# Kernel tuning notes

Measured on AMD Instinct MI355X. Metric: run time of the kernel, lower is better.

The kernel has to match this reference:

```python
import jax, jax.numpy as jnp
import numpy as np

B, T, C, H, NT = 1, 1024, 768, 12, 8
D = C // H  # 64
POWER_ITERS = 4
DP_TEMP = 0.8
ESR_GAMMA = 0.02
ESR_ALPHA = 0.1


def rmsnorm(x, w, eps=1e-6):
    rms = jax.lax.rsqrt(jnp.mean(x * x, axis=-1, keepdims=True) + eps)
    return x * rms * w


def setup_inputs():
    key = jax.random.key(0)
    k0, k1, k2 = jax.random.split(key, 3)
    return {
        "x": jax.random.normal(k0, (B, T, C), jnp.float32),
        "W_qkvg": jax.random.normal(k1, (4 * C, C), jnp.float32) * 0.02,
        "W_out": jax.random.normal(k2, (C, C), jnp.float32) * 0.02,
        "lam": jnp.float32(1.5),
        "log_tau": -0.5 * jnp.ones((H, NT), jnp.float32),
        "logit_w": jnp.zeros((H, NT), jnp.float32),
        "beta": 1.5 * jnp.ones((H,), jnp.float32),
        "out_scale": jnp.ones((H,), jnp.float32),
        "dp_scale": jnp.ones((H,), jnp.float32),
        "logk_scale": jnp.ones((H,), jnp.float32),
        "dt_logit": jnp.float32(np.log(1.0 / 1e-8)),  # dt=1.0 -> logit = log(dt/(1-dt+1e-8))
        "g_norm_w": jnp.ones((D,), jnp.float32),
    }


def reference(x, W_qkvg, W_out, lam, log_tau, logit_w, beta, out_scale,
              dp_scale, logk_scale, dt_logit, g_norm_w):
    # qkvg projection and head split
    qkvg = x @ W_qkvg.T                                    # [B,T,4C]
    q, k, v, g = jnp.split(qkvg, 4, axis=-1)
    to_heads = lambda t: t.reshape(B, T, H, D).transpose(0, 2, 1, 3)  # [B,H,T,D]
    q, k, v, g = map(to_heads, (q, k, v, g))
    g = rmsnorm(g, g_norm_w)

    # pairwise squared distance ||g_i - g_j||^2
    g2 = jnp.sum(g * g, axis=-1)                           # [B,H,T]
    s = jnp.maximum(g2[..., :, None] + g2[..., None, :]
                    - 2.0 * jnp.einsum('bhid,bhjd->bhij', g, g), 0.0)  # [B,H,T,T]

    # fractional log-kernel: logsumexp_t[-(beta/2) log1p(s/(4 tau_t)) + log w_t]
    tau = jnp.maximum(jnp.exp(log_tau), 1e-6)              # [H,NT]
    w = jax.nn.softmax(logit_w, axis=-1)                   # [H,NT]
    beta_c = jnp.clip(beta, 0.5, 2.5)                      # [H]
    log_k_per = -(beta_c[None, :, None, None, None] / 2.0) * jnp.log1p(
        s[:, :, None] / (4.0 * tau[None, :, :, None, None]))          # [B,H,NT,T,T]
    logK = jax.nn.logsumexp(log_k_per + jnp.log(w + 1e-12)[None, :, :, None, None], axis=2)
    logK = logK * logk_scale[None, :, None, None]

    # dot-product scores
    dp = jnp.einsum('bhid,bhjd->bhij', q, k) * (dp_scale[None, :, None, None]
                                                / (np.sqrt(D) * DP_TEMP))

    # causal Markov normalize: blend, mask, stable row-softmax
    mask = jnp.tril(jnp.ones((T, T), bool))[None, None]    # [1,1,T,T]
    blended = lam * dp + (1.0 - lam) * logK
    blended = jnp.where(mask, blended, -jnp.inf)
    mx = jnp.max(blended, axis=-1, keepdims=True)
    mx = jnp.where(jnp.isfinite(mx), mx, 0.0)
    Kmat = jnp.exp(jnp.maximum(blended - mx, -60.0)) * mask
    P = Kmat / jnp.maximum(Kmat.sum(-1, keepdims=True), 1e-12)

    # power iteration for left stationary pi with full-support teleport
    pi0 = jnp.full((B, H, 1, T), 1.0 / T, P.dtype)
    def step(pi, _):
        p = (1.0 - ESR_GAMMA) * (pi @ P) + ESR_GAMMA / T
        p = p / jnp.maximum(p.sum(-1, keepdims=True), 1e-12)
        return p, None
    pi, _ = jax.lax.scan(step, pi0, None, length=POWER_ITERS)
    pi = jax.lax.stop_gradient(pi[..., 0, :])              # [B,H,T] (detached)

    # causal approximation to additive reversibilization
    P_adj = (pi[..., None, :] / jnp.maximum(pi[..., :, None], 1e-12)) \
            * jnp.swapaxes(P, -1, -2)                      # P*_ij = (pi_j/pi_i) P_ji
    P_rev = 0.5 * (P + P_adj) * mask
    P_rev = P_rev / jnp.maximum(P_rev.sum(-1, keepdims=True), 1e-12)

    dt = jax.nn.sigmoid(dt_logit)
    alpha = ESR_ALPHA * dt                                  # scale_alpha_by_dt=True
    P_fin = (1.0 - alpha) * P + alpha * P_rev

    y = (P_fin @ v) * out_scale[None, :, None, None]       # [B,H,T,D]
    y = y.transpose(0, 2, 1, 3).reshape(B, T, C)
    return y @ W_out.T
```

## Files before the change

kernel.cpp:

```cpp
#include <hip/hip_runtime.h>
#include <math.h>

#define TSEQ 1024
#define CD   768
#define HN   12
#define DD   64
#define CH   2

#define OFF_QH     0
#define OFF_KH     393216
#define OFF_GH     786432
#define OFF_VHT    1179648
#define OFF_VH     1572864
#define OFF_G2     1966080
#define OFF_YB     1978368
#define OFF_CONSTS 2371584
#define OFF_OPART  2372096
#define OFF_LS     8663552
#define OFF_PD     8761856
#define OFF_XB     8774144
#define OFF_WQB    9167360
#define OFF_WOB    10347008

#define NG_X  98304
#define NG_WQ 294912
#define NG_WO 73728

typedef __bf16 bf16x8 __attribute__((ext_vector_type(8)));
typedef float  f32x4  __attribute__((ext_vector_type(4)));
typedef unsigned short u16x8 __attribute__((ext_vector_type(8)));
typedef unsigned short u16x4 __attribute__((ext_vector_type(4)));

__device__ inline unsigned short f2bf(float f) {
  unsigned int u = __float_as_uint(f);
  return (unsigned short)((u + 0x7fffu + ((u >> 16) & 1u)) >> 16);
}
__device__ inline float bf2f(unsigned short u) {
  return __uint_as_float((unsigned)u << 16);
}


__global__ __launch_bounds__(256) void convert_kernel(
    const float* __restrict__ x, const float* __restrict__ wq,
    const float* __restrict__ wo, unsigned short* __restrict__ swzA,
    unsigned short* __restrict__ swzWQ, unsigned short* __restrict__ swzWO,
    const float* __restrict__ lam_p, const float* __restrict__ log_tau,
    const float* __restrict__ logit_w, const float* __restrict__ beta,
    const float* __restrict__ out_scale, const float* __restrict__ dp_scale,
    const float* __restrict__ logk_scale, const float* __restrict__ dt_logit,
    float* __restrict__ consts) {
  if (blockIdx.x == 0 && threadIdx.x < 64) {
    int h = threadIdx.x;
    if (h == 0) {
      float dt = 1.0f / (1.0f + __expf(-dt_logit[0]));
      consts[288] = 0.1f * dt;
    }
    if (h < HN) {
      float lam = lam_p[0];
      float* c = consts + h * 24;
      c[0] = lam * dp_scale[h] * (1.0f / 6.4f);
      c[1] = (1.0f - lam) * logk_scale[h];
      float b = fminf(fmaxf(beta[h], 0.5f), 2.5f);
      c[2] = 0.5f * b;
      c[3] = out_scale[h];
      float m = -1e30f;
      float lw[8];
      bool uni = true;
      for (int t = 0; t < 8; t++) {
        lw[t] = logit_w[h * 8 + t];
        m = fmaxf(m, lw[t]);
        if (log_tau[h * 8 + t] != log_tau[h * 8] || lw[t] != lw[0]) uni = false;
      }
      float s = 0.f;
      float e[8];
      for (int t = 0; t < 8; t++) { e[t] = __expf(lw[t] - m); s += e[t]; }
      for (int t = 0; t < 8; t++) {
        float w = e[t] / s;
        c[12 + t] = log2f(w + 1e-12f);
        float tau = fmaxf(__expf(log_tau[h * 8 + t]), 1e-6f);
        c[4 + t] = 1.0f / (4.0f * tau);
      }
      c[20] = uni ? 1.0f : 8.0f;
    }
  }
  int g = blockIdx.x * 256 + threadIdx.x;
  const float* src;
  unsigned short* dst;
  int lg;
  if (g < NG_X) { src = x; dst = swzA; lg = g; }
  else if (g < NG_X + NG_WQ) { src = wq; dst = swzWQ; lg = g - NG_X; }
  else if (g < NG_X + NG_WQ + NG_WO) { src = wo; dst = swzWO; lg = g - NG_X - NG_WQ; }
  else return;
  int lane = lg & 63;
  int kb = (lg >> 6) % 24;
  int t16 = lg / (64 * 24);
  int row = t16 * 16 + (lane & 15);
  int col = kb * 32 + (lane >> 4) * 8;
  const float* s = &src[(size_t)row * 768 + col];
  float4 a = *(const float4*)s;
  float4 b = *(const float4*)(s + 4);
  u16x8 u;
  u[0] = f2bf(a.x); u[1] = f2bf(a.y); u[2] = f2bf(a.z); u[3] = f2bf(a.w);
  u[4] = f2bf(b.x); u[5] = f2bf(b.y); u[6] = f2bf(b.z); u[7] = f2bf(b.w);
  *(u16x8*)&dst[(size_t)lg * 8] = u;
}

__global__ __launch_bounds__(256) void gemm_frag_qkvg(
    const unsigned short* __restrict__ swzA, const unsigned short* __restrict__ swzB,
    const float* __restrict__ consts, const float* __restrict__ g_norm_w,
    unsigned short* __restrict__ qh, unsigned short* __restrict__ kh,
    unsigned short* __restrict__ gh, unsigned short* __restrict__ vh,
    unsigned short* __restrict__ vhT, float* __restrict__ g2) {
  __shared__ __align__(16) unsigned short Ls[64 * 72];
  int t = threadIdx.x, lane = t & 63, w = t >> 6;
  int quad = lane >> 4, tx = lane & 15;
  int bid = blockIdx.x;
  int c = (bid & 7) * 96 + (bid >> 3);
  int ntile = c >> 4;
  int ybk = c & 15;
  int nt0 = ntile * 4;
  int mt0 = ybk * 4 + w;
  int mrow0 = mt0 * 16;

  f32x4 acc[4] = {};
#pragma unroll 4
  for (int kb = 0; kb < 24; kb++) {
    bf16x8 a0 = *(const bf16x8*)&swzA[((size_t)(mt0 * 24 + kb) * 64 + lane) * 8];
#pragma unroll
    for (int ni = 0; ni < 4; ni++) {
      bf16x8 b = *(const bf16x8*)&swzB[((size_t)((nt0 + ni) * 24 + kb) * 64 + lane) * 8];
      acc[ni] = __builtin_amdgcn_mfma_f32_16x16x32_bf16(a0, b, acc[ni], 0, 0, 0);
    }
  }

  int typ = ntile / 12;
  int h = ntile % 12;
  unsigned short* Lw = Ls + w * (16 * 72);

  if (typ == 3) {
    float gw4[4];
#pragma unroll
    for (int ni = 0; ni < 4; ni++) gw4[ni] = g_norm_w[ni * 16 + tx];
#pragma unroll
    for (int reg = 0; reg < 4; reg++) {
      float s1 = acc[0][reg] * acc[0][reg] + acc[1][reg] * acc[1][reg]
               + acc[2][reg] * acc[2][reg] + acc[3][reg] * acc[3][reg];
#pragma unroll
      for (int m = 1; m < 16; m <<= 1) s1 += __shfl_xor(s1, m, 64);
      float rms = rsqrtf(s1 * (1.f / 64.f) + 1e-6f);
      int rl = quad * 4 + reg;
      float s2 = 0.f;
#pragma unroll
      for (int ni = 0; ni < 4; ni++) {
        float v = acc[ni][reg] * rms * gw4[ni];
        unsigned short us = f2bf(v);
        Lw[rl * 72 + ni * 16 + tx] = us;
        float vb = bf2f(us);
        s2 += vb * vb;
      }
#pragma unroll
      for (int m = 1; m < 16; m <<= 1) s2 += __shfl_xor(s2, m, 64);
      if (tx == 0) g2[h * 1024 + mrow0 + rl] = s2;
    }
#pragma unroll
    for (int rep = 0; rep < 2; rep++) {
      int idx = rep * 64 + lane;
      int r = idx >> 3, cc = (idx & 7) * 8;
      *(u16x8*)&gh[(size_t)(h * 1024 + mrow0 + r) * 64 + cc] = *(const u16x8*)&Lw[r * 72 + cc];
    }
  } else {
    float sc = (typ == 0) ? consts[h * 24] * 1.44269504089f : 1.0f;
#pragma unroll
    for (int ni = 0; ni < 4; ni++)
#pragma unroll
      for (int reg = 0; reg < 4; reg++) {
        int rl = quad * 4 + reg;
        Lw[rl * 72 + ni * 16 + tx] = f2bf(acc[ni][reg] * sc);
      }
    unsigned short* dst = (typ == 0) ? qh : ((typ == 1) ? kh : vh);
#pragma unroll
    for (int rep = 0; rep < 2; rep++) {
      int idx = rep * 64 + lane;
      int r = idx >> 3, cc = (idx & 7) * 8;
      *(u16x8*)&dst[(size_t)(h * 1024 + mrow0 + r) * 64 + cc] = *(const u16x8*)&Lw[r * 72 + cc];
    }
    if (typ == 2) {
#pragma unroll
      for (int rep = 0; rep < 2; rep++) {
        int idx = rep * 64 + lane;
        int d = idx >> 1, rc = (idx & 1) * 8;
        u16x8 u;
#pragma unroll
        for (int j = 0; j < 8; j++) u[j] = Lw[(rc + j) * 72 + d];
        *(u16x8*)&vhT[(size_t)(h * 64 + d) * 1024 + mrow0 + rc] = u;
      }
    }
  }
}

__global__ __launch_bounds__(256) void gemm_frag_out(
    const unsigned short* __restrict__ swzA, const unsigned short* __restrict__ swzB,
    float* __restrict__ Cm) {
  int t = threadIdx.x, lane = t & 63, w = t >> 6;
  int quad = lane >> 4, tx = lane & 15;
  int n0 = blockIdx.x * 32;
  int nt0 = blockIdx.x * 2;
  int mt0 = blockIdx.y * 4 + w;

  f32x4 acc[2] = {};
#pragma unroll 4
  for (int kb = 0; kb < 24; kb++) {
    bf16x8 a0 = *(const bf16x8*)&swzA[((size_t)(mt0 * 24 + kb) * 64 + lane) * 8];
#pragma unroll
    for (int ni = 0; ni < 2; ni++) {
      bf16x8 b = *(const bf16x8*)&swzB[((size_t)((nt0 + ni) * 24 + kb) * 64 + lane) * 8];
      acc[ni] = __builtin_amdgcn_mfma_f32_16x16x32_bf16(a0, b, acc[ni], 0, 0, 0);
    }
  }
#pragma unroll
  for (int ni = 0; ni < 2; ni++)
#pragma unroll
    for (int reg = 0; reg < 4; reg++) {
      int row = mt0 * 16 + quad * 4 + reg;
      Cm[(size_t)row * CD + n0 + ni * 16 + tx] = acc[ni][reg];
    }
}

__global__ __launch_bounds__(256, 4) void flash_kernel(
    const unsigned short* __restrict__ qh, const unsigned short* __restrict__ kh,
    const unsigned short* __restrict__ gh, const unsigned short* __restrict__ vhT,
    const float* __restrict__ g2, const float* __restrict__ consts,
    float* __restrict__ Opart, float* __restrict__ lsp, float* __restrict__ pdp) {
  int bid = blockIdx.x;
  int cc0 = (bid & 7) * 108 + (bid >> 3);
  int h = cc0 / 72;
  int uu = 71 - (cc0 % 72);
  int it = 0, rem = uu;
  for (it = 0; it < 16; ++it) {
    int nc = (it + 2) >> 1;
    if (rem < nc) break;
    rem -= nc;
  }
  int njt = it + 1;
  int jt0 = rem * CH;
  int jt1 = (jt0 + CH < njt) ? (jt0 + CH) : njt;
  bool owns_diag = (jt1 == njt);
  int i0 = it * 64;
  int t = threadIdx.x;
  int lane = t & 63, w = t >> 6;
  int quad = lane >> 4, tx = lane & 15;

  __shared__ __align__(16) unsigned short Ks[64 * 72];
  __shared__ __align__(16) unsigned short Gjs[64 * 72];
  __shared__ __align__(16) unsigned short Vt[64 * 72];
  __shared__ __align__(16) __bf16 psh[64 * 72];
  __shared__ float g2i[64], g2j[64], pdiag[64];

  const float* ch = consts + h * 24;
  float lkc = ch[1], bh2 = ch[2];
  int ntt = (int)ch[20];
  float i4t0 = ch[4];
  float cfold = -lkc * bh2;
  float m2i4 = -2.0f * i4t0;
  float g2s = (ntt == 1) ? i4t0 : 1.0f;

  int r4 = t >> 2, cb = (t & 3) * 16;
  int rowb = w * 16 + quad * 4;

  u16x8 pk0, pk1, pg0, pg1, pv0, pv1;
  float pg2 = 0.f;
  {
    int j0 = jt0 * 64;
    const unsigned short* kp = &kh[(size_t)(h * 1024 + j0 + r4) * 64 + cb];
    const unsigned short* gp = &gh[(size_t)(h * 1024 + j0 + r4) * 64 + cb];
    const unsigned short* vp = &vhT[(size_t)(h * 64 + r4) * 1024 + j0 + cb];
    pk0 = *(const u16x8*)kp; pk1 = *(const u16x8*)(kp + 8);
    pg0 = *(const u16x8*)gp; pg1 = *(const u16x8*)(gp + 8);
    pv0 = *(const u16x8*)vp; pv1 = *(const u16x8*)(vp + 8);
    if (t < 64) pg2 = g2[h * 1024 + j0 + t];
  }

  {
    const unsigned short* qp = &qh[(size_t)(h * 1024 + i0 + r4) * 64 + cb];
    const unsigned short* gp = &gh[(size_t)(h * 1024 + i0 + r4) * 64 + cb];
    *(u16x8*)&Ks[r4 * 72 + cb] = *(const u16x8*)qp;
    *(u16x8*)&Ks[r4 * 72 + cb + 8] = *(const u16x8*)(qp + 8);
    *(u16x8*)&Gjs[r4 * 72 + cb] = *(const u16x8*)gp;
    *(u16x8*)&Gjs[r4 * 72 + cb + 8] = *(const u16x8*)(gp + 8);
  }
  if (t < 64) { g2i[t] = g2[h * 1024 + i0 + t]; pdiag[t] = 0.f; }
  __syncthreads();

  bf16x8 aq[2], ag[2];
#pragma unroll
  for (int ks = 0; ks < 2; ks++) {
    aq[ks] = *(const bf16x8*)&Ks[(w * 16 + tx) * 72 + ks * 32 + quad * 8];
    ag[ks] = *(const bf16x8*)&Gjs[(w * 16 + tx) * 72 + ks * 32 + quad * 8];
  }
  float g2i1r[4];
#pragma unroll
  for (int reg = 0; reg < 4; reg++)
    g2i1r[reg] = fmaf(g2i[rowb + reg], i4t0, 1.0f);

  __bf16 onebf = (__bf16)((tx == 0) ? 1.0f : 0.0f);
  bf16x8 bones = {onebf, onebf, onebf, onebf, onebf, onebf, onebf, onebf};

  f32x4 Oc[4] = {};
  f32x4 Osum = {};

  for (int jt = jt0; jt < jt1; jt++) {
    int j0 = jt * 64;
    bool masked = (jt == njt - 1);
    __syncthreads();
    *(u16x8*)&Ks[r4 * 72 + cb] = pk0;
    *(u16x8*)&Ks[r4 * 72 + cb + 8] = pk1;
    *(u16x8*)&Gjs[r4 * 72 + cb] = pg0;
    *(u16x8*)&Gjs[r4 * 72 + cb + 8] = pg1;
    *(u16x8*)&Vt[r4 * 72 + cb] = pv0;
    *(u16x8*)&Vt[r4 * 72 + cb + 8] = pv1;
    if (t < 64) g2j[t] = pg2 * g2s;
    __syncthreads();

    if (jt + 1 < jt1) {
      int jn = j0 + 64;
      const unsigned short* kp = &kh[(size_t)(h * 1024 + jn + r4) * 64 + cb];
      const unsigned short* gp = &gh[(size_t)(h * 1024 + jn + r4) * 64 + cb];
      const unsigned short* vp = &vhT[(size_t)(h * 64 + r4) * 1024 + jn + cb];
      pk0 = *(const u16x8*)kp; pk1 = *(const u16x8*)(kp + 8);
      pg0 = *(const u16x8*)gp; pg1 = *(const u16x8*)(gp + 8);
      pv0 = *(const u16x8*)vp; pv1 = *(const u16x8*)(vp + 8);
      if (t < 64) pg2 = g2[h * 1024 + jn + t];
    }

#pragma unroll
    for (int half = 0; half < 2; half++) {
      f32x4 sqk[2] = {}, sgg[2] = {};
      __builtin_amdgcn_s_setprio(1);
#pragma unroll
      for (int nt2 = 0; nt2 < 2; nt2++) {
        int nt = half * 2 + nt2;
#pragma unroll
        for (int ks = 0; ks < 2; ks++) {
          bf16x8 bk = *(const bf16x8*)&Ks[(nt * 16 + tx) * 72 + ks * 32 + quad * 8];
          sqk[nt2] = __builtin_amdgcn_mfma_f32_16x16x32_bf16(aq[ks], bk, sqk[nt2], 0, 0, 0);
          bf16x8 bg = *(const bf16x8*)&Gjs[(nt * 16 + tx) * 72 + ks * 32 + quad * 8];
          sgg[nt2] = __builtin_amdgcn_mfma_f32_16x16x32_bf16(ag[ks], bg, sgg[nt2], 0, 0, 0);
        }
      }
      __builtin_amdgcn_s_setprio(0);

#pragma unroll
      for (int nt2 = 0; nt2 < 2; nt2++) {
        int nt = half * 2 + nt2;
        float g2jv = g2j[nt * 16 + tx];
        if (ntt == 1) {
#pragma unroll
          for (int reg = 0; reg < 4; reg++) {
            int rowl = rowb + reg;
            float a = fmaxf(fmaf(m2i4, sgg[nt2][reg], g2jv + g2i1r[reg]), 1.0f);
            float lv = __builtin_amdgcn_logf(a);
            float b = fmaf(cfold, lv, sqk[nt2][reg]);
            float p = __builtin_amdgcn_exp2f(b);
            if (masked) {
              int colg = j0 + nt * 16 + tx;
              int gi = i0 + rowl;
              if (colg > gi) p = 0.0f;
              if (colg == gi) pdiag[rowl] = p;
            }
            psh[rowl * 72 + nt * 16 + tx] = (__bf16)p;
          }
        } else {
#pragma unroll
          for (int reg = 0; reg < 4; reg++) {
            int rowl = rowb + reg;
            float s = fmaxf(g2i[rowl] + g2jv - 2.0f * sgg[nt2][reg], 0.0f);
            float se = 0.f;
#pragma unroll
            for (int tt = 0; tt < 8; tt++) {
              float lv = __builtin_amdgcn_logf(fmaf(s, ch[4 + tt], 1.0f));
              se += __builtin_amdgcn_exp2f(fmaf(-bh2, lv, ch[12 + tt]));
            }
            float lse2 = __builtin_amdgcn_logf(se + 1e-30f);
            float b = fmaf(lkc, lse2, sqk[nt2][reg]);
            float p = __builtin_amdgcn_exp2f(b);
            if (masked) {
              int colg = j0 + nt * 16 + tx;
              int gi = i0 + rowl;
              if (colg > gi) p = 0.0f;
              if (colg == gi) pdiag[rowl] = p;
            }
            psh[rowl * 72 + nt * 16 + tx] = (__bf16)p;
          }
        }
      }
    }
    bf16x8 ap[2];
#pragma unroll
    for (int ks = 0; ks < 2; ks++)
      ap[ks] = *(const bf16x8*)&psh[(w * 16 + tx) * 72 + ks * 32 + quad * 8];
    __builtin_amdgcn_s_setprio(1);
#pragma unroll
    for (int nd = 0; nd < 4; nd++) {
#pragma unroll
      for (int ks = 0; ks < 2; ks++) {
        bf16x8 bv = *(const bf16x8*)&Vt[(nd * 16 + tx) * 72 + ks * 32 + quad * 8];
        Oc[nd] = __builtin_amdgcn_mfma_f32_16x16x32_bf16(ap[ks], bv, Oc[nd], 0, 0, 0);
      }
    }
#pragma unroll
    for (int ks = 0; ks < 2; ks++)
      Osum = __builtin_amdgcn_mfma_f32_16x16x32_bf16(ap[ks], bones, Osum, 0, 0, 0);
    __builtin_amdgcn_s_setprio(0);
  }

  if (tx == 0) {
#pragma unroll
    for (int reg = 0; reg < 4; reg++)
      lsp[(size_t)(rem * HN + h) * 1024 + i0 + rowb + reg] = Osum[reg];
  }
  float* Ob = Opart + (size_t)((rem * HN + h) * 1024 + i0) * 64;
#pragma unroll
  for (int nd = 0; nd < 4; nd++) {
#pragma unroll
    for (int reg = 0; reg < 4; reg++) {
      Ob[(rowb + reg) * 64 + nd * 16 + tx] = Oc[nd][reg];
    }
  }
  if (owns_diag) {
    __syncthreads();
    if (t < 64) pdp[h * 1024 + i0 + t] = pdiag[t];
  }
}

__global__ __launch_bounds__(256) void finalize_kernel(
    const float* __restrict__ Opart, const float* __restrict__ lsp,
    const float* __restrict__ pdp, const unsigned short* __restrict__ vh,
    const float* __restrict__ consts, unsigned short* __restrict__ yb) {
  int h = blockIdx.y;
  int t = threadIdx.x;
  int rl = t >> 4, d4 = t & 15;
  int gi = blockIdx.x * 16 + rl;
  int it = gi >> 6;
  int njt = it + 1;
  int nc = (njt + CH - 1) / CH;
  float alpha = consts[288];
  float osc = consts[h * 24 + 3];
  float4 Ov = make_float4(0.f, 0.f, 0.f, 0.f);
  float l = 0.f;
  for (int c = 0; c < nc; c++) {
    float4 p = *(const float4*)&Opart[(size_t)((c * HN + h) * 1024 + gi) * 64 + 4 * d4];
    Ov.x += p.x; Ov.y += p.y; Ov.z += p.z; Ov.w += p.w;
    l += lsp[(size_t)(c * HN + h) * 1024 + gi];
  }
  l = fmaxf(l, 1e-12f);
  float Pii = pdp[h * TSEQ + gi] / l;
  float inv1p = 1.0f / (1.0f + Pii);
  float c1 = (1.0f - alpha) + alpha * inv1p;
  float c2 = alpha * Pii * inv1p;
  float invl = 1.0f / l;
  u16x4 vb = *(const u16x4*)&vh[(size_t)(h * 1024 + gi) * 64 + 4 * d4];
  u16x4 o;
  o[0] = f2bf(osc * (c1 * Ov.x * invl + c2 * bf2f(vb[0])));
  o[1] = f2bf(osc * (c1 * Ov.y * invl + c2 * bf2f(vb[1])));
  o[2] = f2bf(osc * (c1 * Ov.z * invl + c2 * bf2f(vb[2])));
  o[3] = f2bf(osc * (c1 * Ov.w * invl + c2 * bf2f(vb[3])));
  int k = h * 64 + 4 * d4;
  int kb = k >> 5, q8 = (k & 31) >> 3, j0 = k & 7;
  int mt = gi >> 4, txl = gi & 15;
  size_t off = (((size_t)mt * 24 + kb) * 64 + q8 * 16 + txl) * 8 + j0;
  *(u16x4*)&yb[off] = o;
}

extern "C" void kernel_launch(void* const* d_in, const int* in_sizes, int n_in,
                              void* d_out, int out_size, void* d_ws, size_t ws_size,
                              hipStream_t stream) {
  (void)in_sizes; (void)n_in; (void)out_size; (void)ws_size;
  const float* x          = (const float*)d_in[0];
  const float* W_qkvg     = (const float*)d_in[1];
  const float* W_out      = (const float*)d_in[2];
  const float* lam        = (const float*)d_in[3];
  const float* log_tau    = (const float*)d_in[4];
  const float* logit_w    = (const float*)d_in[5];
  const float* beta       = (const float*)d_in[6];
  const float* out_scale  = (const float*)d_in[7];
  const float* dp_scale   = (const float*)d_in[8];
  const float* logk_scale = (const float*)d_in[9];
  const float* dt_logit   = (const float*)d_in[10];
  const float* g_norm_w   = (const float*)d_in[11];
  float* ws = (float*)d_ws;
  unsigned short* qh  = (unsigned short*)(ws + OFF_QH);
  unsigned short* kh  = (unsigned short*)(ws + OFF_KH);
  unsigned short* gh  = (unsigned short*)(ws + OFF_GH);
  unsigned short* vhT = (unsigned short*)(ws + OFF_VHT);
  unsigned short* vh  = (unsigned short*)(ws + OFF_VH);
  float* g2     = ws + OFF_G2;
  unsigned short* yb  = (unsigned short*)(ws + OFF_YB);
  float* consts = ws + OFF_CONSTS;
  float* Opart  = ws + OFF_OPART;
  float* lsp    = ws + OFF_LS;
  float* pdp    = ws + OFF_PD;
  unsigned short* swzA = (unsigned short*)(ws + OFF_XB);
  unsigned short* swzWQ = (unsigned short*)(ws + OFF_WQB);
  unsigned short* swzWO = (unsigned short*)(ws + OFF_WOB);
  float* out = (float*)d_out;

  convert_kernel<<<dim3((NG_X + NG_WQ + NG_WO) / 256), dim3(256), 0, stream>>>(
      x, W_qkvg, W_out, swzA, swzWQ, swzWO,
      lam, log_tau, logit_w, beta, out_scale, dp_scale, logk_scale, dt_logit, consts);
  gemm_frag_qkvg<<<dim3(768), dim3(256), 0, stream>>>(swzA, swzWQ, consts, g_norm_w,
                                                      qh, kh, gh, vh, vhT, g2);
  flash_kernel<<<dim3(864), dim3(256), 0, stream>>>(qh, kh, gh, vhT, g2, consts,
                                                    Opart, lsp, pdp);
  finalize_kernel<<<dim3(64, 12), dim3(256), 0, stream>>>(Opart, lsp, pdp, vh, consts, yb);
  gemm_frag_out<<<dim3(24, 16), dim3(256), 0, stream>>>(yb, swzWO, out);
}
```

Baseline: 143.4 us.

## Fuse finalize into flash kernel via last-block atomic counter reduction

Removes the separate finalize kernel launch. Each flash block increments a per-(head, row-tile) counter after writing its partial outputs, and the last block to arrive reduces all chunk partials and writes the bf16 output tile for the out-projection GEMM. Counters are zeroed in the convert kernel. This saves a launch and its tail, at the cost of atomics, thread fences and a serial reduction tail inside the flash blocks.

```diff
diff --git a/kernel.cpp b/kernel.cpp
--- a/kernel.cpp
+++ b/kernel.cpp
@@ -21,6 +21,7 @@
 #define OFF_XB     8774144
 #define OFF_WQB    9167360
 #define OFF_WOB    10347008
+#define OFF_CNT    10641920
 
 #define NG_X  98304
 #define NG_WQ 294912
@@ -48,7 +49,7 @@
     const float* __restrict__ logit_w, const float* __restrict__ beta,
     const float* __restrict__ out_scale, const float* __restrict__ dp_scale,
     const float* __restrict__ logk_scale, const float* __restrict__ dt_logit,
-    float* __restrict__ consts) {
+    float* __restrict__ consts, int* __restrict__ cnt) {
   if (blockIdx.x == 0 && threadIdx.x < 64) {
     int h = threadIdx.x;
     if (h == 0) {
@@ -82,6 +83,10 @@
       }
       c[20] = uni ? 1.0f : 8.0f;
     }
+  }
+  if (blockIdx.x == 0 && threadIdx.x >= 64) {
+    int i = (int)threadIdx.x - 64;
+    if (i < HN * 16) cnt[i] = 0;
   }
   int g = blockIdx.x * 256 + threadIdx.x;
   const float* src;
@@ -230,7 +235,9 @@
     const unsigned short* __restrict__ qh, const unsigned short* __restrict__ kh,
     const unsigned short* __restrict__ gh, const unsigned short* __restrict__ vhT,
     const float* __restrict__ g2, const float* __restrict__ consts,
-    float* __restrict__ Opart, float* __restrict__ lsp, float* __restrict__ pdp) {
+    float* __restrict__ Opart, float* __restrict__ lsp, float* __restrict__ pdp,
+    const unsigned short* __restrict__ vh, unsigned short* __restrict__ yb,
+    int* __restrict__ cnt) {
   int bid = blockIdx.x;
   int cc0 = (bid & 7) * 108 + (bid >> 3);
   int h = cc0 / 72;
@@ -430,45 +437,50 @@
     __syncthreads();
     if (t < 64) pdp[h * 1024 + i0 + t] = pdiag[t];
   }
-}
-
-__global__ __launch_bounds__(256) void finalize_kernel(
-    const float* __restrict__ Opart, const float* __restrict__ lsp,
-    const float* __restrict__ pdp, const unsigned short* __restrict__ vh,
-    const float* __restrict__ consts, unsigned short* __restrict__ yb) {
-  int h = blockIdx.y;
-  int t = threadIdx.x;
-  int rl = t >> 4, d4 = t & 15;
-  int gi = blockIdx.x * 16 + rl;
-  int it = gi >> 6;
-  int njt = it + 1;
-  int nc = (njt + CH - 1) / CH;
+
+  int ncch = (it + 2) >> 1;
+  __shared__ int lastflag;
+  __syncthreads();
+  if (t == 0) {
+    __threadfence();
+    int prev = atomicAdd(&cnt[h * 16 + it], 1);
+    lastflag = (prev == ncch - 1) ? 1 : 0;
+  }
+  __syncthreads();
+  if (lastflag == 0) return;
+  __threadfence();
+
   float alpha = consts[288];
-  float osc = consts[h * 24 + 3];
-  float4 Ov = make_float4(0.f, 0.f, 0.f, 0.f);
-  float l = 0.f;
-  for (int c = 0; c < nc; c++) {
-    float4 p = *(const float4*)&Opart[(size_t)((c * HN + h) * 1024 + gi) * 64 + 4 * d4];
-    Ov.x += p.x; Ov.y += p.y; Ov.z += p.z; Ov.w += p.w;
-    l += lsp[(size_t)(c * HN + h) * 1024 + gi];
-  }
-  l = fmaxf(l, 1e-12f);
-  float Pii = pdp[h * TSEQ + gi] / l;
-  float inv1p = 1.0f / (1.0f + Pii);
-  float c1 = (1.0f - alpha) + alpha * inv1p;
-  float c2 = alpha * Pii * inv1p;
-  float invl = 1.0f / l;
-  u16x4 vb = *(const u16x4*)&vh[(size_t)(h * 1024 + gi) * 64 + 4 * d4];
-  u16x4 o;
-  o[0] = f2bf(osc * (c1 * Ov.x * invl + c2 * bf2f(vb[0])));
-  o[1] = f2bf(osc * (c1 * Ov.y * invl + c2 * bf2f(vb[1])));
-  o[2] = f2bf(osc * (c1 * Ov.z * invl + c2 * bf2f(vb[2])));
-  o[3] = f2bf(osc * (c1 * Ov.w * invl + c2 * bf2f(vb[3])));
-  int k = h * 64 + 4 * d4;
-  int kb = k >> 5, q8 = (k & 31) >> 3, j0 = k & 7;
-  int mt = gi >> 4, txl = gi & 15;
-  size_t off = (((size_t)mt * 24 + kb) * 64 + q8 * 16 + txl) * 8 + j0;
-  *(u16x4*)&yb[off] = o;
+  float osc = ch[3];
+  int d4 = t & 15, rl0 = t >> 4;
+#pragma unroll
+  for (int pass = 0; pass < 4; pass++) {
+    int gi = i0 + pass * 16 + rl0;
+    float4 Ov = make_float4(0.f, 0.f, 0.f, 0.f);
+    float l = 0.f;
+    for (int c = 0; c < ncch; c++) {
+      float4 p = *(const float4*)&Opart[(size_t)((c * HN + h) * 1024 + gi) * 64 + 4 * d4];
+      Ov.x += p.x; Ov.y += p.y; Ov.z += p.z; Ov.w += p.w;
+      l += lsp[(size_t)(c * HN + h) * 1024 + gi];
+    }
+    l = fmaxf(l, 1e-12f);
+    float Pii = pdp[h * TSEQ + gi] / l;
+    float inv1p = 1.0f / (1.0f + Pii);
+    float c1 = (1.0f - alpha) + alpha * inv1p;
+    float c2 = alpha * Pii * inv1p;
+    float invl = 1.0f / l;
+    u16x4 vb = *(const u16x4*)&vh[(size_t)(h * 1024 + gi) * 64 + 4 * d4];
+    u16x4 o;
+    o[0] = f2bf(osc * (c1 * Ov.x * invl + c2 * bf2f(vb[0])));
+    o[1] = f2bf(osc * (c1 * Ov.y * invl + c2 * bf2f(vb[1])));
+    o[2] = f2bf(osc * (c1 * Ov.z * invl + c2 * bf2f(vb[2])));
+    o[3] = f2bf(osc * (c1 * Ov.w * invl + c2 * bf2f(vb[3])));
+    int k = h * 64 + 4 * d4;
+    int kb2 = k >> 5, q8 = (k & 31) >> 3, j02 = k & 7;
+    int mt = gi >> 4, txl = gi & 15;
+    size_t off = (((size_t)mt * 24 + kb2) * 64 + q8 * 16 + txl) * 8 + j02;
+    *(u16x4*)&yb[off] = o;
+  }
 }
 
 extern "C" void kernel_launch(void* const* d_in, const int* in_sizes, int n_in,
@@ -502,15 +514,16 @@
   unsigned short* swzA = (unsigned short*)(ws + OFF_XB);
   unsigned short* swzWQ = (unsigned short*)(ws + OFF_WQB);
   unsigned short* swzWO = (unsigned short*)(ws + OFF_WOB);
+  int* cnt = (int*)(ws + OFF_CNT);
   float* out = (float*)d_out;
 
   convert_kernel<<<dim3((NG_X + NG_WQ + NG_WO) / 256), dim3(256), 0, stream>>>(
       x, W_qkvg, W_out, swzA, swzWQ, swzWO,
-      lam, log_tau, logit_w, beta, out_scale, dp_scale, logk_scale, dt_logit, consts);
+      lam, log_tau, logit_w, beta, out_scale, dp_scale, logk_scale, dt_logit,
+      consts, cnt);
   gemm_frag_qkvg<<<dim3(768), dim3(256), 0, stream>>>(swzA, swzWQ, consts, g_norm_w,
                                                       qh, kh, gh, vh, vhT, g2);
   flash_kernel<<<dim3(864), dim3(256), 0, stream>>>(qh, kh, gh, vhT, g2, consts,
-                                                    Opart, lsp, pdp);
-  finalize_kernel<<<dim3(64, 12), dim3(256), 0, stream>>>(Opart, lsp, pdp, vh, consts, yb);
+                                                    Opart, lsp, pdp, vh, yb, cnt);
   gemm_frag_out<<<dim3(24, 16), dim3(256), 0, stream>>>(yb, swzWO, out);
 }
```

Result: slower. 194.3 us (+35.5%).
